# Performance work log

Measured on AMD Instinct MI355X. Metric: run time of the kernel, lower is better.

## Reference

```python
import jax, jax.numpy as jnp
import numpy as np

N_NODES = 100000
N_EDGES = 1600000
D_FEAT = 32


def setup_inputs() -> dict:
    key = jax.random.key(0)
    k1, k2, k3 = jax.random.split(key, 3)
    x = jax.random.normal(k1, (N_NODES, D_FEAT), dtype=jnp.float32)
    a = jax.random.randint(k2, (2, N_EDGES), 0, N_NODES, dtype=jnp.int64)
    e = jax.random.normal(k3, (N_EDGES,), dtype=jnp.float32)
    return {"x": x, "a": a, "e": e}


def reference(x, a, e):
    # phi: per-edge message = x[src] * e  (scalar edge weight)
    # sigma: per-target-node sum of incoming messages (0 for isolated nodes)
    src = a[0]
    tgt = a[1]
    msgs = x[src] * e[:, None]                       # [n_edges, d]
    out = jax.ops.segment_sum(msgs, tgt, num_segments=x.shape[0])  # [n_nodes, d]
    return out
```

## Files before the change

kernel.cpp:

```cpp
#include <hip/hip_runtime.h>
#include <hip/hip_bf16.h>


#define D_FEAT   32
#define SHIFT    7
#define BNODES   128
#define CHUNK    8192
#define MAXNB    1024
#define CAP      4096

__global__ void zero_out_kernel(float* __restrict__ out, int n) {
    int i = blockIdx.x * blockDim.x + threadIdx.x;
    if (i < n) out[i] = 0.0f;
}

__global__ void scatter_add_kernel(const float* __restrict__ x,
                                   const int* __restrict__ src,
                                   const int* __restrict__ tgt,
                                   const float* __restrict__ e,
                                   float* __restrict__ out,
                                   int n_edges) {
    long long gid   = (long long)blockIdx.x * blockDim.x + threadIdx.x;
    long long total = (long long)n_edges * D_FEAT;
    if (gid >= total) return;
    int edge = (int)(gid >> 5);
    int f    = (int)(gid & 31);
    float m = x[(long long)src[edge] * D_FEAT + f] * e[edge];
    atomicAdd(&out[(long long)tgt[edge] * D_FEAT + f], m);
}


__global__ __launch_bounds__(1024) void p1_hist_kernel(
        const int* __restrict__ tgt, int* __restrict__ Hg,
        int n_edges, int NB, int nchunks) {
    __shared__ int cnt[MAXNB];
    for (int i = threadIdx.x; i < NB; i += 1024) cnt[i] = 0;
    __syncthreads();
    int base = blockIdx.x * CHUNK;
    int lim  = min(base + CHUNK, n_edges);
    for (int i = base + threadIdx.x; i < lim; i += 1024)
        atomicAdd(&cnt[tgt[i] >> SHIFT], 1);
    __syncthreads();
    for (int i = threadIdx.x; i < NB; i += 1024)
        Hg[i * nchunks + blockIdx.x] = cnt[i];
}

__global__ void scan_block_kernel(int* __restrict__ data, int* __restrict__ bsum,
                                  int n) {
    __shared__ int s[256];
    int i = blockIdx.x * 256 + threadIdx.x;
    int v = (i < n) ? data[i] : 0;
    s[threadIdx.x] = v;
    __syncthreads();
    #pragma unroll
    for (int d = 1; d < 256; d <<= 1) {
        int t = (threadIdx.x >= d) ? s[threadIdx.x - d] : 0;
        __syncthreads();
        s[threadIdx.x] += t;
        __syncthreads();
    }
    if (i < n) data[i] = s[threadIdx.x] - v;
    if (threadIdx.x == 255) bsum[blockIdx.x] = s[255];
}

__global__ void scan_bsum_kernel(int* __restrict__ bsum, int nblk) {
    __shared__ int s[1024];
    int tid = threadIdx.x;
    int v = (tid < nblk) ? bsum[tid] : 0;
    s[tid] = v;
    __syncthreads();
    for (int d = 1; d < 1024; d <<= 1) {
        int t = (tid >= d) ? s[tid - d] : 0;
        __syncthreads();
        s[tid] += t;
        __syncthreads();
    }
    if (tid < nblk) bsum[tid] = s[tid] - v;
}

__global__ void add_base_kernel(int* __restrict__ data, const int* __restrict__ bsum,
                                int n) {
    int i = blockIdx.x * 256 + threadIdx.x;
    if (i < n) data[i] += bsum[blockIdx.x];
}

__global__ __launch_bounds__(1024) void p1_scatter_kernel(
        const int* __restrict__ src,
        const int* __restrict__ tgt,
        const float* __restrict__ e,
        const int* __restrict__ Hg,
        int2* __restrict__ rec,
        int n_edges, int NB, int nchunks) {
    __shared__ int cur[MAXNB];
    for (int i = threadIdx.x; i < NB; i += 1024)
        cur[i] = Hg[i * nchunks + blockIdx.x];
    __syncthreads();
    int base = blockIdx.x * CHUNK;
    int lim  = min(base + CHUNK, n_edges);
    for (int i = base + threadIdx.x; i < lim; i += 1024) {
        int t = tgt[i];
        int b = t >> SHIFT;
        int pos = atomicAdd(&cur[b], 1);
        rec[pos] = make_int2(src[i] | ((t & (BNODES - 1)) << 17),
                             __float_as_int(e[i]));
    }
}

__global__ __launch_bounds__(1024) void p2_apply_kernel(
        const float* __restrict__ x, const int2* __restrict__ rec,
        const int* __restrict__ Hg, float* __restrict__ out,
        int n_edges, int n_nodes, int NB, int nchunks) {
    __shared__ int2 srt[CAP];
    __shared__ int  cnt[BNODES];
    __shared__ int  off[BNODES + 1];
    __shared__ int  cur[BNODES];
    __shared__ int  stmp[BNODES];

    int tid  = threadIdx.x;
    int b    = blockIdx.x;
    int base = Hg[b * nchunks];
    int end  = (b + 1 < NB) ? Hg[(b + 1) * nchunks] : n_edges;
    int nrec = end - base;

    if (nrec <= CAP) {
        if (tid < BNODES) cnt[tid] = 0;
        __syncthreads();
        for (int r = base + tid; r < end; r += 1024) {
            int2 a = rec[r];
            atomicAdd(&cnt[(a.x >> 17) & (BNODES - 1)], 1);
        }
        __syncthreads();
        int v = (tid < BNODES) ? cnt[tid] : 0;
        if (tid < BNODES) stmp[tid] = v;
        __syncthreads();
        #pragma unroll
        for (int d = 1; d < BNODES; d <<= 1) {
            int t = (tid < BNODES && tid >= d) ? stmp[tid - d] : 0;
            __syncthreads();
            if (tid < BNODES) stmp[tid] += t;
            __syncthreads();
        }
        if (tid < BNODES) { off[tid] = stmp[tid] - v; cur[tid] = stmp[tid] - v; }
        if (tid == 0) off[BNODES] = nrec;
        __syncthreads();
        for (int r = base + tid; r < end; r += 1024) {
            int2 a = rec[r];
            int pos = atomicAdd(&cur[(a.x >> 17) & (BNODES - 1)], 1);
            srt[pos] = a;
        }
        __syncthreads();
        int f = tid & 31;
        int g = tid >> 5;
        for (int ln = g; ln < BNODES; ln += 32) {
            int p  = off[ln];
            int pe = off[ln + 1];
            float acc = 0.0f;
            for (; p + 3 < pe; p += 4) {
                int2 r0 = srt[p];
                int2 r1 = srt[p + 1];
                int2 r2 = srt[p + 2];
                int2 r3 = srt[p + 3];
                float v0 = x[(r0.x & 0x1FFFF) * D_FEAT + f] * __int_as_float(r0.y);
                float v1 = x[(r1.x & 0x1FFFF) * D_FEAT + f] * __int_as_float(r1.y);
                float v2 = x[(r2.x & 0x1FFFF) * D_FEAT + f] * __int_as_float(r2.y);
                float v3 = x[(r3.x & 0x1FFFF) * D_FEAT + f] * __int_as_float(r3.y);
                acc += (v0 + v1) + (v2 + v3);
            }
            for (; p < pe; ++p) {
                int2 r0 = srt[p];
                acc += x[(r0.x & 0x1FFFF) * D_FEAT + f] * __int_as_float(r0.y);
            }
            int node = (b << SHIFT) + ln;
            if (node < n_nodes)
                out[(long long)node * D_FEAT + f] = acc;
        }
    } else {
        float* accS = (float*)srt;
        for (int i = tid; i < BNODES * D_FEAT; i += 1024) accS[i] = 0.0f;
        __syncthreads();
        int f = tid & 31;
        for (int r = base + (tid >> 5); r < end; r += 32) {
            int2 a = rec[r];
            float v = x[(a.x & 0x1FFFF) * D_FEAT + f] * __int_as_float(a.y);
            atomicAdd(&accS[((a.x >> 17) & (BNODES - 1)) * D_FEAT + f], v);
        }
        __syncthreads();
        int out0 = b << SHIFT;
        for (int i = tid; i < BNODES * D_FEAT; i += 1024) {
            int node = out0 + (i >> 5);
            if (node < n_nodes) out[(long long)out0 * D_FEAT + i] = accS[i];
        }
    }
}

extern "C" void kernel_launch(void* const* d_in, const int* in_sizes, int n_in,
                              void* d_out, int out_size, void* d_ws, size_t ws_size,
                              hipStream_t stream) {
    const float* x = (const float*)d_in[0];
    const int*   a = (const int*)d_in[1];
    const float* e = (const float*)d_in[2];

    int n_edges = in_sizes[2];
    int n_nodes = out_size / D_FEAT;
    const int* src = a;
    const int* tgt = a + n_edges;
    float* out = (float*)d_out;

    int NB        = (n_nodes + BNODES - 1) >> SHIFT;
    int nchunks   = (n_edges + CHUNK - 1) / CHUNK;
    int scan_n    = NB * nchunks;
    int nblk_scan = (scan_n + 255) / 256;

    size_t rec_bytes  = (size_t)n_edges * sizeof(int2);
    size_t hg_bytes   = (size_t)scan_n * sizeof(int);
    size_t bsum_bytes = (size_t)nblk_scan * sizeof(int);
    size_t need = rec_bytes + hg_bytes + bsum_bytes;

    bool ok = (ws_size >= need) && (NB <= MAXNB) && (nblk_scan <= 1024) &&
              (n_nodes <= (1 << 17));
    if (!ok) {
        int threads = 256;
        zero_out_kernel<<<(out_size + threads - 1) / threads, threads, 0, stream>>>(out, out_size);
        long long total = (long long)n_edges * D_FEAT;
        int blocks = (int)((total + threads - 1) / threads);
        scatter_add_kernel<<<blocks, threads, 0, stream>>>(x, src, tgt, e, out, n_edges);
        return;
    }

    char* p = (char*)d_ws;
    int2* rec  = (int2*)p; p += rec_bytes;
    int*  Hg   = (int*)p;  p += hg_bytes;
    int*  bsum = (int*)p;

    p1_hist_kernel<<<nchunks, 1024, 0, stream>>>(tgt, Hg, n_edges, NB, nchunks);
    scan_block_kernel<<<nblk_scan, 256, 0, stream>>>(Hg, bsum, scan_n);
    scan_bsum_kernel<<<1, 1024, 0, stream>>>(bsum, nblk_scan);
    add_base_kernel<<<nblk_scan, 256, 0, stream>>>(Hg, bsum, scan_n);
    p1_scatter_kernel<<<nchunks, 1024, 0, stream>>>(src, tgt, e, Hg, rec, n_edges, NB, nchunks);
    p2_apply_kernel<<<NB, 1024, 0, stream>>>(x, rec, Hg, out, n_edges, n_nodes, NB, nchunks);
}
```

Before: 68.91 us.

## Vectorize edge loads, fold scan base-add into consumers, stage records in LDS

Histogram and scatter passes now read src/tgt/e with 128-bit vector loads, processing four edges per thread iteration. The separate add_base launch is removed; consumers add the block-scan offset on the fly. The apply kernel copies its bucket's records into LDS once and sorts 16-bit indices instead of re-reading records from global memory. This adds an extra indirection through LDS and more shared memory per block.

```diff
diff --git a/kernel.cpp b/kernel.cpp
--- a/kernel.cpp
+++ b/kernel.cpp
@@ -38,7 +38,17 @@
     __syncthreads();
     int base = blockIdx.x * CHUNK;
     int lim  = min(base + CHUNK, n_edges);
-    for (int i = base + threadIdx.x; i < lim; i += 1024)
+    int n    = lim - base;
+    int nv   = n >> 2;
+    const int4* t4p = (const int4*)(tgt + base);
+    for (int v = threadIdx.x; v < nv; v += 1024) {
+        int4 t4 = t4p[v];
+        atomicAdd(&cnt[t4.x >> SHIFT], 1);
+        atomicAdd(&cnt[t4.y >> SHIFT], 1);
+        atomicAdd(&cnt[t4.z >> SHIFT], 1);
+        atomicAdd(&cnt[t4.w >> SHIFT], 1);
+    }
+    for (int i = base + (nv << 2) + threadIdx.x; i < lim; i += 1024)
         atomicAdd(&cnt[tgt[i] >> SHIFT], 1);
     __syncthreads();
     for (int i = threadIdx.x; i < NB; i += 1024)
@@ -78,29 +88,43 @@
     if (tid < nblk) bsum[tid] = s[tid] - v;
 }
 
-__global__ void add_base_kernel(int* __restrict__ data, const int* __restrict__ bsum,
-                                int n) {
-    int i = blockIdx.x * 256 + threadIdx.x;
-    if (i < n) data[i] += bsum[blockIdx.x];
-}
-
 __global__ __launch_bounds__(1024) void p1_scatter_kernel(
         const int* __restrict__ src,
         const int* __restrict__ tgt,
         const float* __restrict__ e,
         const int* __restrict__ Hg,
+        const int* __restrict__ bsum,
         int2* __restrict__ rec,
         int n_edges, int NB, int nchunks) {
     __shared__ int cur[MAXNB];
-    for (int i = threadIdx.x; i < NB; i += 1024)
-        cur[i] = Hg[i * nchunks + blockIdx.x];
+    for (int i = threadIdx.x; i < NB; i += 1024) {
+        int j = i * nchunks + blockIdx.x;
+        cur[i] = Hg[j] + bsum[j >> 8];
+    }
     __syncthreads();
     int base = blockIdx.x * CHUNK;
     int lim  = min(base + CHUNK, n_edges);
-    for (int i = base + threadIdx.x; i < lim; i += 1024) {
+    int n    = lim - base;
+    int nv   = n >> 2;
+    const int4*   s4p = (const int4*)(src + base);
+    const int4*   t4p = (const int4*)(tgt + base);
+    const float4* e4p = (const float4*)(e + base);
+    for (int v = threadIdx.x; v < nv; v += 1024) {
+        int4   s4 = s4p[v];
+        int4   t4 = t4p[v];
+        float4 e4 = e4p[v];
+        int p0 = atomicAdd(&cur[t4.x >> SHIFT], 1);
+        int p1 = atomicAdd(&cur[t4.y >> SHIFT], 1);
+        int p2 = atomicAdd(&cur[t4.z >> SHIFT], 1);
+        int p3 = atomicAdd(&cur[t4.w >> SHIFT], 1);
+        rec[p0] = make_int2(s4.x | ((t4.x & (BNODES - 1)) << 17), __float_as_int(e4.x));
+        rec[p1] = make_int2(s4.y | ((t4.y & (BNODES - 1)) << 17), __float_as_int(e4.y));
+        rec[p2] = make_int2(s4.z | ((t4.z & (BNODES - 1)) << 17), __float_as_int(e4.z));
+        rec[p3] = make_int2(s4.w | ((t4.w & (BNODES - 1)) << 17), __float_as_int(e4.w));
+    }
+    for (int i = base + (nv << 2) + threadIdx.x; i < lim; i += 1024) {
         int t = tgt[i];
-        int b = t >> SHIFT;
-        int pos = atomicAdd(&cur[b], 1);
+        int pos = atomicAdd(&cur[t >> SHIFT], 1);
         rec[pos] = make_int2(src[i] | ((t & (BNODES - 1)) << 17),
                              __float_as_int(e[i]));
     }
@@ -108,9 +132,11 @@
 
 __global__ __launch_bounds__(1024) void p2_apply_kernel(
         const float* __restrict__ x, const int2* __restrict__ rec,
-        const int* __restrict__ Hg, float* __restrict__ out,
+        const int* __restrict__ Hg, const int* __restrict__ bsum,
+        float* __restrict__ out,
         int n_edges, int n_nodes, int NB, int nchunks) {
     __shared__ int2 srt[CAP];
+    __shared__ unsigned short sidx[CAP];
     __shared__ int  cnt[BNODES];
     __shared__ int  off[BNODES + 1];
     __shared__ int  cur[BNODES];
@@ -118,15 +144,23 @@
 
     int tid  = threadIdx.x;
     int b    = blockIdx.x;
-    int base = Hg[b * nchunks];
-    int end  = (b + 1 < NB) ? Hg[(b + 1) * nchunks] : n_edges;
+    int j0   = b * nchunks;
+    int base = Hg[j0] + bsum[j0 >> 8];
+    int end;
+    if (b + 1 < NB) {
+        int j1 = (b + 1) * nchunks;
+        end = Hg[j1] + bsum[j1 >> 8];
+    } else {
+        end = n_edges;
+    }
     int nrec = end - base;
 
     if (nrec <= CAP) {
         if (tid < BNODES) cnt[tid] = 0;
         __syncthreads();
-        for (int r = base + tid; r < end; r += 1024) {
-            int2 a = rec[r];
+        for (int r = tid; r < nrec; r += 1024) {
+            int2 a = rec[base + r];
+            srt[r] = a;
             atomicAdd(&cnt[(a.x >> 17) & (BNODES - 1)], 1);
         }
         __syncthreads();
@@ -143,10 +177,10 @@
         if (tid < BNODES) { off[tid] = stmp[tid] - v; cur[tid] = stmp[tid] - v; }
         if (tid == 0) off[BNODES] = nrec;
         __syncthreads();
-        for (int r = base + tid; r < end; r += 1024) {
-            int2 a = rec[r];
-            int pos = atomicAdd(&cur[(a.x >> 17) & (BNODES - 1)], 1);
-            srt[pos] = a;
+        for (int r = tid; r < nrec; r += 1024) {
+            int ln = (srt[r].x >> 17) & (BNODES - 1);
+            int pos = atomicAdd(&cur[ln], 1);
+            sidx[pos] = (unsigned short)r;
         }
         __syncthreads();
         int f = tid & 31;
@@ -156,10 +190,10 @@
             int pe = off[ln + 1];
             float acc = 0.0f;
             for (; p + 3 < pe; p += 4) {
-                int2 r0 = srt[p];
-                int2 r1 = srt[p + 1];
-                int2 r2 = srt[p + 2];
-                int2 r3 = srt[p + 3];
+                int2 r0 = srt[sidx[p]];
+                int2 r1 = srt[sidx[p + 1]];
+                int2 r2 = srt[sidx[p + 2]];
+                int2 r3 = srt[sidx[p + 3]];
                 float v0 = x[(r0.x & 0x1FFFF) * D_FEAT + f] * __int_as_float(r0.y);
                 float v1 = x[(r1.x & 0x1FFFF) * D_FEAT + f] * __int_as_float(r1.y);
                 float v2 = x[(r2.x & 0x1FFFF) * D_FEAT + f] * __int_as_float(r2.y);
@@ -167,7 +201,7 @@
                 acc += (v0 + v1) + (v2 + v3);
             }
             for (; p < pe; ++p) {
-                int2 r0 = srt[p];
+                int2 r0 = srt[sidx[p]];
                 acc += x[(r0.x & 0x1FFFF) * D_FEAT + f] * __int_as_float(r0.y);
             }
             int node = (b << SHIFT) + ln;
@@ -235,7 +269,6 @@
     p1_hist_kernel<<<nchunks, 1024, 0, stream>>>(tgt, Hg, n_edges, NB, nchunks);
     scan_block_kernel<<<nblk_scan, 256, 0, stream>>>(Hg, bsum, scan_n);
     scan_bsum_kernel<<<1, 1024, 0, stream>>>(bsum, nblk_scan);
-    add_base_kernel<<<nblk_scan, 256, 0, stream>>>(Hg, bsum, scan_n);
-    p1_scatter_kernel<<<nchunks, 1024, 0, stream>>>(src, tgt, e, Hg, rec, n_edges, NB, nchunks);
-    p2_apply_kernel<<<NB, 1024, 0, stream>>>(x, rec, Hg, out, n_edges, n_nodes, NB, nchunks);
-}
+    p1_scatter_kernel<<<nchunks, 1024, 0, stream>>>(src, tgt, e, Hg, bsum, rec, n_edges, NB, nchunks);
+    p2_apply_kernel<<<NB, 1024, 0, stream>>>(x, rec, Hg, bsum, out, n_edges, n_nodes, NB, nchunks);
+}
```

Result: slower. 72.54 us (+5.3%).
